# Kernel tuning notes

Measured on AMD Instinct MI355X. Metric: run time of the kernel, lower is better.

## Reference

```python
import jax, jax.numpy as jnp
import numpy as np

N_NODES = 100000
N_EDGES = 1600000
N_GRAPHS = 1000


def _gcn_layer(x, W, b, row, col, dinv):
    # GCNConv with improved=True: A_hat = A + 2I, symmetric normalization.
    xw = x @ W  # [N, out]
    norm = dinv[row] * dinv[col]  # [E]
    agg = jax.ops.segment_sum(norm[:, None] * xw[row], col, num_segments=N_NODES)
    # self-loop contribution with fill weight 2.0
    agg = agg + (2.0 * dinv * dinv)[:, None] * xw
    return agg + b


def setup_inputs() -> dict:
    key = jax.random.key(0)
    ks = jax.random.split(key, 20)
    x = jax.random.normal(ks[0], (N_NODES, 336), dtype=jnp.float32)
    edge_index = jax.random.randint(ks[1], (2, N_EDGES), 0, N_NODES, dtype=jnp.int64)
    batch = jnp.sort(jax.random.randint(ks[2], (N_NODES,), 0, N_GRAPHS, dtype=jnp.int64))
    def lin(k, din, dout):
        s = 1.0 / np.sqrt(din)
        return jax.random.uniform(k, (din, dout), jnp.float32, -s, s)
    params = {
        'W1': lin(ks[3], 336, 100), 'b1': jnp.zeros((100,), jnp.float32),
        'W2': lin(ks[4], 100, 100), 'b2': jnp.zeros((100,), jnp.float32),
        'W3': lin(ks[5], 100, 100), 'b3': jnp.zeros((100,), jnp.float32),
        'W4': lin(ks[6], 100, 100), 'b4': jnp.zeros((100,), jnp.float32),
        'W5': lin(ks[7], 100, 100), 'b5': jnp.zeros((100,), jnp.float32),
        'Wl1': lin(ks[8], 100, 100), 'bl1': jnp.zeros((100,), jnp.float32),
        'Wl2': lin(ks[9], 100, 100), 'bl2': jnp.zeros((100,), jnp.float32),
        'Wl3': lin(ks[10], 100, 29), 'bl3': jnp.zeros((29,), jnp.float32),
    }
    return {'x': x, 'edge_index': edge_index, 'batch': batch, **params}


def reference(x, edge_index, batch, W1, b1, W2, b2, W3, b3, W4, b4, W5, b5,
              Wl1, bl1, Wl2, bl2, Wl3, bl3):
    row, col = edge_index[0], edge_index[1]
    # degree of A + 2I (edge weights are 1, self-loop weight 2)
    deg = jax.ops.segment_sum(jnp.ones((N_EDGES,), x.dtype), col, num_segments=N_NODES) + 2.0
    dinv = deg ** -0.5
    h = jax.nn.relu(_gcn_layer(x, W1, b1, row, col, dinv))
    h = jax.nn.relu(_gcn_layer(h, W2, b2, row, col, dinv))
    h = jax.nn.relu(_gcn_layer(h, W3, b3, row, col, dinv))
    h = jax.nn.relu(_gcn_layer(h, W4, b4, row, col, dinv))
    h = jax.nn.relu(_gcn_layer(h, W5, b5, row, col, dinv))
    # global mean pool over graphs
    sums = jax.ops.segment_sum(h, batch, num_segments=N_GRAPHS)
    counts = jax.ops.segment_sum(jnp.ones((N_NODES,), h.dtype), batch, num_segments=N_GRAPHS)
    pooled = sums / jnp.maximum(counts, 1.0)[:, None]
    g = jax.nn.relu(pooled @ Wl1 + bl1)
    g = jax.nn.relu(g @ Wl2 + bl2)
    return g @ Wl3 + bl3
```

## Files before the change

kernel.cpp:

```cpp
#include <hip/hip_runtime.h>
#include <hip/hip_fp16.h>
#include <stdint.h>

#define NN 100000
#define NE 1600000
#define NG 1000
#define LDA 112
#define LDX 128

#define NPART 8
#define PRANGE 12500
#define SGRID 2048
#define PSTRIDE 65536

typedef float f32x4 __attribute__((ext_vector_type(4)));
typedef _Float16 f16x8 __attribute__((ext_vector_type(8)));

__device__ __forceinline__ void load_lds16(const void* g, void* l) {
    __builtin_amdgcn_global_load_lds((const __attribute__((address_space(1))) unsigned int*)g,
                                     (__attribute__((address_space(3))) unsigned int*)l,
                                     16, 0, 0);
}

__global__ void k_deg(const int* __restrict__ col, int* __restrict__ degcnt) {
    int part = blockIdx.x & (NPART - 1);
    int pb = blockIdx.x >> 3;
    int lo = part * PRANGE, hi = lo + PRANGE;
    for (int e = pb * 256 + threadIdx.x; e < NE; e += PSTRIDE) {
        int c = col[e];
        if (c >= lo && c < hi) atomicAdd(&degcnt[c], 1);
    }
}

__global__ void k_scan1(const int* __restrict__ cnt, int* __restrict__ csum) {
    __shared__ int s[256];
    int i = blockIdx.x * 256 + threadIdx.x;
    s[threadIdx.x] = (i < NN) ? cnt[i] : 0;
    __syncthreads();
    for (int o = 128; o > 0; o >>= 1) {
        if (threadIdx.x < o) s[threadIdx.x] += s[threadIdx.x + o];
        __syncthreads();
    }
    if (threadIdx.x == 0) csum[blockIdx.x] = s[0];
}

__global__ void k_scan2(const int* __restrict__ csum, int* __restrict__ csum2, int nb) {
    __shared__ int s[512];
    int t = threadIdx.x;
    int v = (t < nb) ? csum[t] : 0;
    s[t] = v; __syncthreads();
    for (int o = 1; o < 512; o <<= 1) {
        int x = (t >= o) ? s[t - o] : 0;
        __syncthreads();
        s[t] += x;
        __syncthreads();
    }
    if (t < nb) csum2[t] = s[t] - v;
}

__global__ void k_scan3d(const int* __restrict__ cnt, const int* __restrict__ csum2,
                         int* __restrict__ indptr, float* __restrict__ dinv) {
    __shared__ int s[256];
    int t = threadIdx.x;
    int i = blockIdx.x * 256 + t;
    int v = (i < NN) ? cnt[i] : 0;
    s[t] = v; __syncthreads();
    for (int o = 1; o < 256; o <<= 1) {
        int x = (t >= o) ? s[t - o] : 0;
        __syncthreads();
        s[t] += x;
        __syncthreads();
    }
    if (i < NN) {
        indptr[i] = csum2[blockIdx.x] + s[t] - v;
        dinv[i] = 1.0f / sqrtf((float)v + 2.0f);
    }
    if (i == 0) indptr[NN] = NE;
}

__global__ void k_scatter(const int* __restrict__ row, const int* __restrict__ col,
                          const int* __restrict__ indptr,
                          int* __restrict__ fill, int* __restrict__ esrc) {
    int part = blockIdx.x & (NPART - 1);
    int pb = blockIdx.x >> 3;
    int lo = part * PRANGE, hi = lo + PRANGE;
    for (int e = pb * 256 + threadIdx.x; e < NE; e += PSTRIDE) {
        int c = col[e];
        int r = row[e];
        if (c >= lo && c < hi) {
            int pos = indptr[c] + atomicAdd(&fill[c], 1);
            esrc[pos] = r;
        }
    }
}

__global__ void k_gbounds(const int* __restrict__ batch, int* __restrict__ gstart) {
    int i = blockIdx.x * 256 + threadIdx.x;
    if (i >= NN) return;
    int b = batch[i];
    int pb = (i == 0) ? -1 : batch[i - 1];
    for (int g = pb + 1; g <= b; g++) gstart[g] = i;
    if (i == NN - 1) {
        for (int g = b + 1; g <= NG; g++) gstart[g] = NN;
    }
}

__global__ void k_convW(const float* __restrict__ W1, __half* __restrict__ w1h, __half* __restrict__ w1l,
                        const float* __restrict__ W2, __half* __restrict__ w2h, __half* __restrict__ w2l,
                        const float* __restrict__ W3, __half* __restrict__ w3h, __half* __restrict__ w3l,
                        const float* __restrict__ W4, __half* __restrict__ w4h, __half* __restrict__ w4l,
                        const float* __restrict__ W5, __half* __restrict__ w5h, __half* __restrict__ w5l) {
    int b = blockIdx.x, t = threadIdx.x;
    const float* W; __half *Wh, *Wl; int K, KCP, idx;
    if (b < 168) {
        W = W1; Wh = w1h; Wl = w1l; K = 336; KCP = 384; idx = b * 256 + t;
    } else {
        int li = (b - 168) / 56;
        int lb = (b - 168) % 56;
        const float* Ws[4] = {W2, W3, W4, W5};
        __half* Whs[4] = {w2h, w3h, w4h, w5h};
        __half* Wls[4] = {w2l, w3l, w4l, w5l};
        W = Ws[li]; Wh = Whs[li]; Wl = Wls[li]; K = 100; KCP = 128; idx = lb * 256 + t;
    }
    int n = idx / KCP, k = idx - n * KCP;
    float v = (n < 100 && k < K) ? W[k * 100 + n] : 0.f;
    __half hi = __float2half(v);
    __half lo = __float2half((v - __half2float(hi)) * 2048.f);
    int kc = k & 127;
    size_t so = (size_t)n * KCP + (k - kc) + (kc ^ ((n & 7) << 3));
    Wh[so] = hi;
    Wl[so] = lo;
}

__device__ __forceinline__ f16x8 cvt8(float4 v0, float4 v1) {
    __half2 p0 = __floats2half2_rn(v0.x, v0.y);
    __half2 p1 = __floats2half2_rn(v0.z, v0.w);
    __half2 p2 = __floats2half2_rn(v1.x, v1.y);
    __half2 p3 = __floats2half2_rn(v1.z, v1.w);
    union { uint4 u; f16x8 f; } c;
    c.u.x = __builtin_bit_cast(unsigned, p0);
    c.u.y = __builtin_bit_cast(unsigned, p1);
    c.u.z = __builtin_bit_cast(unsigned, p2);
    c.u.w = __builtin_bit_cast(unsigned, p3);
    return c.f;
}

__global__ __launch_bounds__(512, 2) void k_gemmX(const float* __restrict__ x,
                                                  const __half* __restrict__ Whi,
                                                  const __half* __restrict__ Wlo,
                                                  const float* __restrict__ dinv,
                                                  __half* __restrict__ out) {
    __shared__ __align__(16) __half Hs[2][112 * 128];
    __shared__ __align__(16) __half Ls[2][112 * 128];
    int t = threadIdx.x;
    int lane = t & 63, wv = t >> 6;
    int l15 = lane & 15, quad = lane >> 4;
    int rowbase = blockIdx.x * 128;
    int arow = rowbase + wv * 16 + l15;
    bool arok = arow < NN;
    const float* xp = x + (size_t)arow * 336;

    f32x4 acch[7], accl[7];
#pragma unroll
    for (int i = 0; i < 7; i++)
#pragma unroll
        for (int r = 0; r < 4; r++) { acch[i][r] = 0.f; accl[i][r] = 0.f; }

    int swz = (l15 & 7) << 4;
    float4 araw[8];

    auto stage = [&](int buf, int k0) {
#pragma unroll
        for (int cch = 0; cch < 7; cch++) {
            int g = wv + cch * 8;
            int tb = (g >= 28);
            int o = (g - (tb ? 28 : 0)) * 1024 + lane * 16;
            int r = o >> 8, cc = o & 255;
            size_t src = (size_t)r * 768 + (size_t)(k0 * 2) + cc;
            if (!tb) load_lds16((const char*)Whi + src, (char*)Hs[buf] + o);
            else     load_lds16((const char*)Wlo + src, (char*)Ls[buf] + o);
        }
    };
    auto aload = [&](int k0) {
#pragma unroll
        for (int ks = 0; ks < 4; ks++) {
            int k = k0 + ks * 32 + quad * 8;
            float4 v0 = make_float4(0.f, 0.f, 0.f, 0.f), v1 = v0;
            if (arok && k < 336) {
                v0 = *(const float4*)(xp + k);
                v1 = *(const float4*)(xp + k + 4);
            }
            araw[ks * 2] = v0;
            araw[ks * 2 + 1] = v1;
        }
    };

    stage(0, 0);
    aload(0);

#pragma unroll
    for (int tch = 0; tch < 3; tch++) {
        asm volatile("s_waitcnt vmcnt(0)" ::: "memory");
        f16x8 a[4];
#pragma unroll
        for (int ks = 0; ks < 4; ks++) a[ks] = cvt8(araw[ks * 2], araw[ks * 2 + 1]);
        __builtin_amdgcn_s_barrier();
        __builtin_amdgcn_sched_barrier(0);
        if (tch < 2) {
            aload((tch + 1) * 128);
            stage((tch + 1) & 1, (tch + 1) * 128);
        }
        const char* HB = (const char*)Hs[tch & 1];
        const char* LB = (const char*)Ls[tch & 1];
#pragma unroll
        for (int ks = 0; ks < 4; ks++) {
            int cb = (ks * 64 + quad * 16) ^ swz;
#pragma unroll
            for (int tt = 0; tt < 7; tt++) {
                int ro = (tt * 16 + l15) * 256;
                f16x8 bh = *(const f16x8*)(HB + ro + cb);
                f16x8 bl = *(const f16x8*)(LB + ro + cb);
                acch[tt] = __builtin_amdgcn_mfma_f32_16x16x32_f16(a[ks], bh, acch[tt], 0, 0, 0);
                accl[tt] = __builtin_amdgcn_mfma_f32_16x16x32_f16(a[ks], bl, accl[tt], 0, 0, 0);
            }
        }
        __builtin_amdgcn_sched_barrier(0);
        __builtin_amdgcn_s_barrier();
    }

    int gr0 = rowbase + wv * 16 + quad * 4;
    float dv[4];
#pragma unroll
    for (int reg = 0; reg < 4; reg++) dv[reg] = (gr0 + reg < NN) ? dinv[gr0 + reg] : 0.f;
#pragma unroll
    for (int tt = 0; tt < 7; tt++) {
        int n = tt * 16 + l15;
#pragma unroll
        for (int reg = 0; reg < 4; reg++) {
            int gr = gr0 + reg;
            if (gr < NN)
                out[(size_t)gr * LDX + n] =
                    __float2half(dv[reg] * (acch[tt][reg] + accl[tt][reg] * (1.f / 2048.f)));
        }
    }
    if (l15 < 8) {
#pragma unroll
        for (int reg = 0; reg < 4; reg++) {
            int gr = gr0 + reg;
            if (gr < NN) *(unsigned int*)(out + (size_t)gr * LDX + 112 + l15 * 2) = 0u;
        }
    }
}

__global__ __launch_bounds__(512, 4) void k_gemmH(const __half* __restrict__ act,
                                                  const __half* __restrict__ Whi,
                                                  const __half* __restrict__ Wlo,
                                                  const float* __restrict__ dinv,
                                                  __half* __restrict__ out) {
    __shared__ __align__(16) __half Hs[112 * 128];
    __shared__ __align__(16) __half Ls[112 * 128];
    int t = threadIdx.x;
    int lane = t & 63, wv = t >> 6;
    int l15 = lane & 15, quad = lane >> 4;
    int rowbase = blockIdx.x * 128;
    int ar = min(rowbase + wv * 16 + l15, NN - 1);

    const char* ap = (const char*)act + (size_t)ar * 256;
    f16x8 a[4];
#pragma unroll
    for (int ks = 0; ks < 4; ks++)
        a[ks] = *(const f16x8*)(ap + ks * 64 + quad * 16);

#pragma unroll
    for (int cch = 0; cch < 7; cch++) {
        int g = wv + cch * 8;
        int tb = (g >= 28);
        int o = (g - (tb ? 28 : 0)) * 1024 + lane * 16;
        if (!tb) load_lds16((const char*)Whi + o, (char*)Hs + o);
        else     load_lds16((const char*)Wlo + o, (char*)Ls + o);
    }

    f32x4 acch[7], accl[7];
#pragma unroll
    for (int i = 0; i < 7; i++)
#pragma unroll
        for (int r = 0; r < 4; r++) { acch[i][r] = 0.f; accl[i][r] = 0.f; }

    __syncthreads();
    int swz = (l15 & 7) << 4;
#pragma unroll
    for (int ks = 0; ks < 4; ks++) {
        int cb = (ks * 64 + quad * 16) ^ swz;
#pragma unroll
        for (int tt = 0; tt < 7; tt++) {
            int ro = (tt * 16 + l15) * 256;
            f16x8 bh = *(const f16x8*)((const char*)Hs + ro + cb);
            f16x8 bl = *(const f16x8*)((const char*)Ls + ro + cb);
            acch[tt] = __builtin_amdgcn_mfma_f32_16x16x32_f16(a[ks], bh, acch[tt], 0, 0, 0);
            accl[tt] = __builtin_amdgcn_mfma_f32_16x16x32_f16(a[ks], bl, accl[tt], 0, 0, 0);
        }
    }

    int gr0 = rowbase + wv * 16 + quad * 4;
    float dv[4];
#pragma unroll
    for (int reg = 0; reg < 4; reg++) dv[reg] = (gr0 + reg < NN) ? dinv[gr0 + reg] : 0.f;
#pragma unroll
    for (int tt = 0; tt < 7; tt++) {
        int n = tt * 16 + l15;
#pragma unroll
        for (int reg = 0; reg < 4; reg++) {
            int gr = gr0 + reg;
            if (gr < NN)
                out[(size_t)gr * LDX + n] =
                    __float2half(dv[reg] * (acch[tt][reg] + accl[tt][reg] * (1.f / 2048.f)));
        }
    }
    if (l15 < 8) {
#pragma unroll
        for (int reg = 0; reg < 4; reg++) {
            int gr = gr0 + reg;
            if (gr < NN) *(unsigned int*)(out + (size_t)gr * LDX + 112 + l15 * 2) = 0u;
        }
    }
}

__device__ __forceinline__ void agg_core(const __half* __restrict__ xs,
                                         const int* __restrict__ esrc,
                                         int beg, int end, int lane, int col,
                                         float& ax, float& ay) {
    ax = 0.f; ay = 0.f;
    for (int c = beg; c < end; c += 64) {
        int m = min(64, end - c);
        int se = 0;
        if (lane < m) se = esrc[c + lane];
        int j = 0;
        for (; j + 32 <= m; j += 32) {
            __half2 v[32];
#pragma unroll
            for (int u = 0; u < 32; u++) {
                int s = __builtin_amdgcn_readlane(se, j + u);
                v[u] = *(const __half2*)(xs + (size_t)s * LDX + col);
            }
#pragma unroll
            for (int u = 0; u < 32; u++) {
                float2 f = __half22float2(v[u]);
                ax += f.x; ay += f.y;
            }
        }
        for (; j + 16 <= m; j += 16) {
            __half2 v[16];
#pragma unroll
            for (int u = 0; u < 16; u++) {
                int s = __builtin_amdgcn_readlane(se, j + u);
                v[u] = *(const __half2*)(xs + (size_t)s * LDX + col);
            }
#pragma unroll
            for (int u = 0; u < 16; u++) {
                float2 f = __half22float2(v[u]);
                ax += f.x; ay += f.y;
            }
        }
        for (; j + 8 <= m; j += 8) {
            __half2 v[8];
#pragma unroll
            for (int u = 0; u < 8; u++) {
                int s = __builtin_amdgcn_readlane(se, j + u);
                v[u] = *(const __half2*)(xs + (size_t)s * LDX + col);
            }
#pragma unroll
            for (int u = 0; u < 8; u++) {
                float2 f = __half22float2(v[u]);
                ax += f.x; ay += f.y;
            }
        }
        for (; j + 4 <= m; j += 4) {
            __half2 v[4];
#pragma unroll
            for (int u = 0; u < 4; u++) {
                int s = __builtin_amdgcn_readlane(se, j + u);
                v[u] = *(const __half2*)(xs + (size_t)s * LDX + col);
            }
#pragma unroll
            for (int u = 0; u < 4; u++) {
                float2 f = __half22float2(v[u]);
                ax += f.x; ay += f.y;
            }
        }
        for (; j < m; j++) {
            int s = __builtin_amdgcn_readlane(se, j);
            float2 f = __half22float2(*(const __half2*)(xs + (size_t)s * LDX + col));
            ax += f.x; ay += f.y;
        }
    }
}

__global__ __launch_bounds__(256) void k_aggS(const __half* __restrict__ xs,
                                              const int* __restrict__ indptr,
                                              const int* __restrict__ esrc,
                                              const float* __restrict__ dinv,
                                              const float* __restrict__ bias,
                                              __half* __restrict__ hh) {
    int wave = threadIdx.x >> 6;
    int lane = threadIdx.x & 63;
    int n = blockIdx.x * 4 + wave;
    if (n >= NN) return;
    int beg = indptr[n], end = indptr[n + 1];
    int col = (lane < 50) ? lane * 2 : 0;
    float ax, ay;
    agg_core(xs, esrc, beg, end, lane, col, ax, ay);
    if (lane < 50) {
        float di = dinv[n];
        float2 xv = __half22float2(*(const __half2*)(xs + (size_t)n * LDX + col));
        float2 bv = *(const float2*)(bias + lane * 2);
        float hx = fmaxf(di * (ax + 2.f * xv.x) + bv.x, 0.f);
        float hy = fmaxf(di * (ay + 2.f * xv.y) + bv.y, 0.f);
        *(__half2*)(hh + (size_t)n * LDX + col) = __floats2half2_rn(hx, hy);
    } else {
        int pc = 100 + (lane - 50) * 2;
        *(unsigned int*)(hh + (size_t)n * LDX + pc) = 0u;
    }
}

__global__ __launch_bounds__(256) void k_agg(const __half* __restrict__ xs,
                                             const int* __restrict__ indptr,
                                             const int* __restrict__ esrc,
                                             const float* __restrict__ dinv,
                                             const float* __restrict__ bias,
                                             float* __restrict__ hout) {
    int wave = threadIdx.x >> 6;
    int lane = threadIdx.x & 63;
    int n = blockIdx.x * 4 + wave;
    if (n >= NN) return;
    int beg = indptr[n], end = indptr[n + 1];
    int col = (lane < 50) ? lane * 2 : 0;
    float ax, ay;
    agg_core(xs, esrc, beg, end, lane, col, ax, ay);
    if (lane < 50) {
        float di = dinv[n];
        float2 xv = __half22float2(*(const __half2*)(xs + (size_t)n * LDX + col));
        float2 bv = *(const float2*)(bias + lane * 2);
        float2 r;
        r.x = fmaxf(di * (ax + 2.f * xv.x) + bv.x, 0.f);
        r.y = fmaxf(di * (ay + 2.f * xv.y) + bv.y, 0.f);
        *(float2*)(hout + (size_t)n * LDA + col) = r;
    }
}

__global__ __launch_bounds__(128) void k_pool(const float* __restrict__ h,
                                              const int* __restrict__ gstart,
                                              float* __restrict__ pooled) {
    int g = blockIdx.x, t = threadIdx.x;
    if (t >= 100) return;
    int st = gstart[g];
    int cnt = gstart[g + 1] - st;
    float s0 = 0.f, s1 = 0.f, s2 = 0.f, s3 = 0.f;
    float s4 = 0.f, s5 = 0.f, s6 = 0.f, s7 = 0.f;
    int i = 0;
    for (; i + 8 <= cnt; i += 8) {
        s0 += h[(size_t)(st + i) * LDA + t];
        s1 += h[(size_t)(st + i + 1) * LDA + t];
        s2 += h[(size_t)(st + i + 2) * LDA + t];
        s3 += h[(size_t)(st + i + 3) * LDA + t];
        s4 += h[(size_t)(st + i + 4) * LDA + t];
        s5 += h[(size_t)(st + i + 5) * LDA + t];
        s6 += h[(size_t)(st + i + 6) * LDA + t];
        s7 += h[(size_t)(st + i + 7) * LDA + t];
    }
    for (; i < cnt; i++) s0 += h[(size_t)(st + i) * LDA + t];
    float s = ((s0 + s1) + (s2 + s3)) + ((s4 + s5) + (s6 + s7));
    pooled[g * 100 + t] = s / (float)(cnt > 0 ? cnt : 1);
}

__global__ void k_mlp(const float* __restrict__ pooled,
                      const float* __restrict__ Wl1, const float* __restrict__ bl1,
                      const float* __restrict__ Wl2, const float* __restrict__ bl2,
                      const float* __restrict__ Wl3, const float* __restrict__ bl3,
                      float* __restrict__ out) {
    __shared__ float p[100], q[100];
    int g = blockIdx.x, t = threadIdx.x;
    if (t < 100) p[t] = pooled[g * 100 + t];
    __syncthreads();
    float s1 = 0.f;
    if (t < 100) {
        s1 = bl1[t];
        for (int k = 0; k < 100; k++) s1 += p[k] * Wl1[k * 100 + t];
        s1 = fmaxf(s1, 0.f);
    }
    __syncthreads();
    if (t < 100) q[t] = s1;
    __syncthreads();
    float s2 = 0.f;
    if (t < 100) {
        s2 = bl2[t];
        for (int k = 0; k < 100; k++) s2 += q[k] * Wl2[k * 100 + t];
        s2 = fmaxf(s2, 0.f);
    }
    __syncthreads();
    if (t < 100) p[t] = s2;
    __syncthreads();
    if (t < 29) {
        float s3 = bl3[t];
        for (int k = 0; k < 100; k++) s3 += p[k] * Wl3[k * 29 + t];
        out[g * 29 + t] = s3;
    }
}

extern "C" void kernel_launch(void* const* d_in, const int* in_sizes, int n_in,
                              void* d_out, int out_size, void* d_ws, size_t ws_size,
                              hipStream_t stream) {
    const float* x     = (const float*)d_in[0];
    const int*   ei    = (const int*)d_in[1];
    const int*   batch = (const int*)d_in[2];
    const float* W1 = (const float*)d_in[3];  const float* b1 = (const float*)d_in[4];
    const float* W2 = (const float*)d_in[5];  const float* b2 = (const float*)d_in[6];
    const float* W3 = (const float*)d_in[7];  const float* b3 = (const float*)d_in[8];
    const float* W4 = (const float*)d_in[9];  const float* b4 = (const float*)d_in[10];
    const float* W5 = (const float*)d_in[11]; const float* b5 = (const float*)d_in[12];
    const float* Wl1 = (const float*)d_in[13]; const float* bl1 = (const float*)d_in[14];
    const float* Wl2 = (const float*)d_in[15]; const float* bl2 = (const float*)d_in[16];
    const float* Wl3 = (const float*)d_in[17]; const float* bl3 = (const float*)d_in[18];
    float* out = (float*)d_out;

    const int* row = ei;
    const int* col = ei + NE;

    uintptr_t base = (uintptr_t)d_ws;
    auto alloc = [&](size_t bytes) -> void* {
        void* p = (void*)base;
        base += (bytes + 255) & ~(size_t)255;
        return p;
    };
    int*   cnts   = (int*)alloc((size_t)(2 * NN) * 4);
    int*   degcnt = cnts;
    int*   fill   = cnts + NN;
    float* dinv   = (float*)alloc(NN * 4);
    int*   indptr = (int*)alloc((NN + 1) * 4);
    int*   csum   = (int*)alloc(512 * 4);
    int*   csum2  = (int*)alloc(512 * 4);
    int*   gstart = (int*)alloc((NG + 1) * 4);
    int*   esrc   = (int*)alloc((size_t)NE * 4);
    __half* xsh   = (__half*)alloc((size_t)NN * LDX * 2);
    __half* hh    = (__half*)alloc((size_t)NN * LDX * 2);
    float* h      = (float*)alloc((size_t)NN * LDA * 4);
    float* pooled = (float*)alloc((size_t)NG * 100 * 4);
    __half* w1hi = (__half*)alloc((size_t)112 * 384 * 2);
    __half* w1lo = (__half*)alloc((size_t)112 * 384 * 2);
    __half* w2hi = (__half*)alloc((size_t)112 * 128 * 2);
    __half* w2lo = (__half*)alloc((size_t)112 * 128 * 2);
    __half* w3hi = (__half*)alloc((size_t)112 * 128 * 2);
    __half* w3lo = (__half*)alloc((size_t)112 * 128 * 2);
    __half* w4hi = (__half*)alloc((size_t)112 * 128 * 2);
    __half* w4lo = (__half*)alloc((size_t)112 * 128 * 2);
    __half* w5hi = (__half*)alloc((size_t)112 * 128 * 2);
    __half* w5lo = (__half*)alloc((size_t)112 * 128 * 2);

    hipMemsetAsync(cnts, 0, (size_t)(2 * NN) * 4, stream);

    const int NB = (NN + 255) / 256;
    k_deg<<<SGRID, 256, 0, stream>>>(col, degcnt);
    k_scan1<<<NB, 256, 0, stream>>>(degcnt, csum);
    k_scan2<<<1, 512, 0, stream>>>(csum, csum2, NB);
    k_scan3d<<<NB, 256, 0, stream>>>(degcnt, csum2, indptr, dinv);
    k_scatter<<<SGRID, 256, 0, stream>>>(row, col, indptr, fill, esrc);
    k_gbounds<<<NB, 256, 0, stream>>>(batch, gstart);
    k_convW<<<392, 256, 0, stream>>>(W1, w1hi, w1lo, W2, w2hi, w2lo,
                                     W3, w3hi, w3lo, W4, w4hi, w4lo,
                                     W5, w5hi, w5lo);

    const int GEMM_GRID = (NN + 127) / 128;
    const int AGG_GRID = (NN + 3) / 4;

    k_gemmX<<<GEMM_GRID, 512, 0, stream>>>(x, w1hi, w1lo, dinv, xsh);
    k_aggS<<<AGG_GRID, 256, 0, stream>>>(xsh, indptr, esrc, dinv, b1, hh);
    k_gemmH<<<GEMM_GRID, 512, 0, stream>>>(hh, w2hi, w2lo, dinv, xsh);
    k_aggS<<<AGG_GRID, 256, 0, stream>>>(xsh, indptr, esrc, dinv, b2, hh);
    k_gemmH<<<GEMM_GRID, 512, 0, stream>>>(hh, w3hi, w3lo, dinv, xsh);
    k_aggS<<<AGG_GRID, 256, 0, stream>>>(xsh, indptr, esrc, dinv, b3, hh);
    k_gemmH<<<GEMM_GRID, 512, 0, stream>>>(hh, w4hi, w4lo, dinv, xsh);
    k_aggS<<<AGG_GRID, 256, 0, stream>>>(xsh, indptr, esrc, dinv, b4, hh);
    k_gemmH<<<GEMM_GRID, 512, 0, stream>>>(hh, w5hi, w5lo, dinv, xsh);
    k_agg<<<AGG_GRID, 256, 0, stream>>>(xsh, indptr, esrc, dinv, b5, h);

    k_pool<<<NG, 128, 0, stream>>>(h, gstart, pooled);
    k_mlp<<<NG, 128, 0, stream>>>(pooled, Wl1, bl1, Wl2, bl2, Wl3, bl3, out);
}
```

Before: 835.5 us.

## Shrink weight tiles to 100 rows and drop double buffering to raise GEMM occupancy

Stores the transposed hi/lo fp16 weight tiles with 100 output rows instead of 112 padded rows, shrinking LDS per block. B-fragment reads clamp row indices past 99 and zero those output columns. k_gemmX drops its double-buffered LDS staging in favour of a single buffer loaded each K chunk, with a partial vmcnt wait so the next x chunk prefetches during compute. Launch bounds rise to 4 and 6 blocks per SM, aiming for more resident waves, at the cost of losing weight-load/compute overlap in k_gemmX and possibly more register pressure.

```diff
diff --git a/kernel.cpp b/kernel.cpp
--- a/kernel.cpp
+++ b/kernel.cpp
@@ -112,18 +112,18 @@
                         const float* __restrict__ W5, __half* __restrict__ w5h, __half* __restrict__ w5l) {
     int b = blockIdx.x, t = threadIdx.x;
     const float* W; __half *Wh, *Wl; int K, KCP, idx;
-    if (b < 168) {
+    if (b < 150) {
         W = W1; Wh = w1h; Wl = w1l; K = 336; KCP = 384; idx = b * 256 + t;
     } else {
-        int li = (b - 168) / 56;
-        int lb = (b - 168) % 56;
+        int li = (b - 150) / 50;
+        int lb = (b - 150) % 50;
         const float* Ws[4] = {W2, W3, W4, W5};
         __half* Whs[4] = {w2h, w3h, w4h, w5h};
         __half* Wls[4] = {w2l, w3l, w4l, w5l};
         W = Ws[li]; Wh = Whs[li]; Wl = Wls[li]; K = 100; KCP = 128; idx = lb * 256 + t;
     }
     int n = idx / KCP, k = idx - n * KCP;
-    float v = (n < 100 && k < K) ? W[k * 100 + n] : 0.f;
+    float v = (k < K) ? W[k * 100 + n] : 0.f;
     __half hi = __float2half(v);
     __half lo = __float2half((v - __half2float(hi)) * 2048.f);
     int kc = k & 127;
@@ -145,13 +145,13 @@
     return c.f;
 }
 
-__global__ __launch_bounds__(512, 2) void k_gemmX(const float* __restrict__ x,
+__global__ __launch_bounds__(512, 4) void k_gemmX(const float* __restrict__ x,
                                                   const __half* __restrict__ Whi,
                                                   const __half* __restrict__ Wlo,
                                                   const float* __restrict__ dinv,
                                                   __half* __restrict__ out) {
-    __shared__ __align__(16) __half Hs[2][112 * 128];
-    __shared__ __align__(16) __half Ls[2][112 * 128];
+    __shared__ __align__(16) __half Hs[100 * 128];
+    __shared__ __align__(16) __half Ls[100 * 128];
     int t = threadIdx.x;
     int lane = t & 63, wv = t >> 6;
     int l15 = lane & 15, quad = lane >> 4;
@@ -169,16 +169,18 @@
     int swz = (l15 & 7) << 4;
     float4 araw[8];
 
-    auto stage = [&](int buf, int k0) {
-#pragma unroll
-        for (int cch = 0; cch < 7; cch++) {
-            int g = wv + cch * 8;
-            int tb = (g >= 28);
-            int o = (g - (tb ? 28 : 0)) * 1024 + lane * 16;
-            int r = o >> 8, cc = o & 255;
-            size_t src = (size_t)r * 768 + (size_t)(k0 * 2) + cc;
-            if (!tb) load_lds16((const char*)Whi + src, (char*)Hs[buf] + o);
-            else     load_lds16((const char*)Wlo + src, (char*)Ls[buf] + o);
+    auto stage = [&](int k0) {
+#pragma unroll
+        for (int i = 0; i < 7; i++) {
+            int g = wv + i * 8;
+            if (g < 50) {
+                int tb = (g >= 25);
+                int o = (g - (tb ? 25 : 0)) * 1024 + lane * 16;
+                int r = o >> 8, cc = o & 255;
+                size_t src = (size_t)r * 768 + (size_t)(k0 * 2) + cc;
+                if (!tb) load_lds16((const char*)Whi + src, (char*)Hs + o);
+                else     load_lds16((const char*)Wlo + src, (char*)Ls + o);
+            }
         }
     };
     auto aload = [&](int k0) {
@@ -195,31 +197,33 @@
         }
     };
 
-    stage(0, 0);
     aload(0);
 
 #pragma unroll
     for (int tch = 0; tch < 3; tch++) {
-        asm volatile("s_waitcnt vmcnt(0)" ::: "memory");
+        stage(tch * 128);
         f16x8 a[4];
 #pragma unroll
         for (int ks = 0; ks < 4; ks++) a[ks] = cvt8(araw[ks * 2], araw[ks * 2 + 1]);
+        if (tch < 2) {
+            aload((tch + 1) * 128);
+            asm volatile("s_waitcnt vmcnt(8)" ::: "memory");
+        } else {
+            asm volatile("s_waitcnt vmcnt(0)" ::: "memory");
+        }
+        __builtin_amdgcn_sched_barrier(0);
         __builtin_amdgcn_s_barrier();
         __builtin_amdgcn_sched_barrier(0);
-        if (tch < 2) {
-            aload((tch + 1) * 128);
-            stage((tch + 1) & 1, (tch + 1) * 128);
-        }
-        const char* HB = (const char*)Hs[tch & 1];
-        const char* LB = (const char*)Ls[tch & 1];
 #pragma unroll
         for (int ks = 0; ks < 4; ks++) {
             int cb = (ks * 64 + quad * 16) ^ swz;
 #pragma unroll
             for (int tt = 0; tt < 7; tt++) {
-                int ro = (tt * 16 + l15) * 256;
-                f16x8 bh = *(const f16x8*)(HB + ro + cb);
-                f16x8 bl = *(const f16x8*)(LB + ro + cb);
+                int nrow = tt * 16 + l15;
+                int nr = (nrow > 99) ? 99 : nrow;
+                int ro = nr * 256;
+                f16x8 bh = *(const f16x8*)((const char*)Hs + ro + cb);
+                f16x8 bl = *(const f16x8*)((const char*)Ls + ro + cb);
                 acch[tt] = __builtin_amdgcn_mfma_f32_16x16x32_f16(a[ks], bh, acch[tt], 0, 0, 0);
                 accl[tt] = __builtin_amdgcn_mfma_f32_16x16x32_f16(a[ks], bl, accl[tt], 0, 0, 0);
             }
@@ -238,9 +242,10 @@
 #pragma unroll
         for (int reg = 0; reg < 4; reg++) {
             int gr = gr0 + reg;
-            if (gr < NN)
-                out[(size_t)gr * LDX + n] =
-                    __float2half(dv[reg] * (acch[tt][reg] + accl[tt][reg] * (1.f / 2048.f)));
+            if (gr < NN) {
+                float v = dv[reg] * (acch[tt][reg] + accl[tt][reg] * (1.f / 2048.f));
+                out[(size_t)gr * LDX + n] = (n < 100) ? __float2half(v) : __half(0.f);
+            }
         }
     }
     if (l15 < 8) {
@@ -252,13 +257,13 @@
     }
 }
 
-__global__ __launch_bounds__(512, 4) void k_gemmH(const __half* __restrict__ act,
+__global__ __launch_bounds__(512, 6) void k_gemmH(const __half* __restrict__ act,
                                                   const __half* __restrict__ Whi,
                                                   const __half* __restrict__ Wlo,
                                                   const float* __restrict__ dinv,
                                                   __half* __restrict__ out) {
-    __shared__ __align__(16) __half Hs[112 * 128];
-    __shared__ __align__(16) __half Ls[112 * 128];
+    __shared__ __align__(16) __half Hs[100 * 128];
+    __shared__ __align__(16) __half Ls[100 * 128];
     int t = threadIdx.x;
     int lane = t & 63, wv = t >> 6;
     int l15 = lane & 15, quad = lane >> 4;
@@ -272,12 +277,14 @@
         a[ks] = *(const f16x8*)(ap + ks * 64 + quad * 16);
 
 #pragma unroll
-    for (int cch = 0; cch < 7; cch++) {
-        int g = wv + cch * 8;
-        int tb = (g >= 28);
-        int o = (g - (tb ? 28 : 0)) * 1024 + lane * 16;
-        if (!tb) load_lds16((const char*)Whi + o, (char*)Hs + o);
-        else     load_lds16((const char*)Wlo + o, (char*)Ls + o);
+    for (int i = 0; i < 7; i++) {
+        int g = wv + i * 8;
+        if (g < 50) {
+            int tb = (g >= 25);
+            int o = (g - (tb ? 25 : 0)) * 1024 + lane * 16;
+            if (!tb) load_lds16((const char*)Whi + o, (char*)Hs + o);
+            else     load_lds16((const char*)Wlo + o, (char*)Ls + o);
+        }
     }
 
     f32x4 acch[7], accl[7];
@@ -293,7 +300,9 @@
         int cb = (ks * 64 + quad * 16) ^ swz;
 #pragma unroll
         for (int tt = 0; tt < 7; tt++) {
-            int ro = (tt * 16 + l15) * 256;
+            int nrow = tt * 16 + l15;
+            int nr = (nrow > 99) ? 99 : nrow;
+            int ro = nr * 256;
             f16x8 bh = *(const f16x8*)((const char*)Hs + ro + cb);
             f16x8 bl = *(const f16x8*)((const char*)Ls + ro + cb);
             acch[tt] = __builtin_amdgcn_mfma_f32_16x16x32_f16(a[ks], bh, acch[tt], 0, 0, 0);
@@ -311,9 +320,10 @@
 #pragma unroll
         for (int reg = 0; reg < 4; reg++) {
             int gr = gr0 + reg;
-            if (gr < NN)
-                out[(size_t)gr * LDX + n] =
-                    __float2half(dv[reg] * (acch[tt][reg] + accl[tt][reg] * (1.f / 2048.f)));
+            if (gr < NN) {
+                float v = dv[reg] * (acch[tt][reg] + accl[tt][reg] * (1.f / 2048.f));
+                out[(size_t)gr * LDX + n] = (n < 100) ? __float2half(v) : __half(0.f);
+            }
         }
     }
     if (l15 < 8) {
@@ -544,16 +554,16 @@
     __half* hh    = (__half*)alloc((size_t)NN * LDX * 2);
     float* h      = (float*)alloc((size_t)NN * LDA * 4);
     float* pooled = (float*)alloc((size_t)NG * 100 * 4);
-    __half* w1hi = (__half*)alloc((size_t)112 * 384 * 2);
-    __half* w1lo = (__half*)alloc((size_t)112 * 384 * 2);
-    __half* w2hi = (__half*)alloc((size_t)112 * 128 * 2);
-    __half* w2lo = (__half*)alloc((size_t)112 * 128 * 2);
-    __half* w3hi = (__half*)alloc((size_t)112 * 128 * 2);
-    __half* w3lo = (__half*)alloc((size_t)112 * 128 * 2);
-    __half* w4hi = (__half*)alloc((size_t)112 * 128 * 2);
-    __half* w4lo = (__half*)alloc((size_t)112 * 128 * 2);
-    __half* w5hi = (__half*)alloc((size_t)112 * 128 * 2);
-    __half* w5lo = (__half*)alloc((size_t)112 * 128 * 2);
+    __half* w1hi = (__half*)alloc((size_t)100 * 384 * 2);
+    __half* w1lo = (__half*)alloc((size_t)100 * 384 * 2);
+    __half* w2hi = (__half*)alloc((size_t)100 * 128 * 2);
+    __half* w2lo = (__half*)alloc((size_t)100 * 128 * 2);
+    __half* w3hi = (__half*)alloc((size_t)100 * 128 * 2);
+    __half* w3lo = (__half*)alloc((size_t)100 * 128 * 2);
+    __half* w4hi = (__half*)alloc((size_t)100 * 128 * 2);
+    __half* w4lo = (__half*)alloc((size_t)100 * 128 * 2);
+    __half* w5hi = (__half*)alloc((size_t)100 * 128 * 2);
+    __half* w5lo = (__half*)alloc((size_t)100 * 128 * 2);
 
     hipMemsetAsync(cnts, 0, (size_t)(2 * NN) * 4, stream);
 
@@ -564,7 +574,7 @@
     k_scan3d<<<NB, 256, 0, stream>>>(degcnt, csum2, indptr, dinv);
     k_scatter<<<SGRID, 256, 0, stream>>>(row, col, indptr, fill, esrc);
     k_gbounds<<<NB, 256, 0, stream>>>(batch, gstart);
-    k_convW<<<392, 256, 0, stream>>>(W1, w1hi, w1lo, W2, w2hi, w2lo,
+    k_convW<<<350, 256, 0, stream>>>(W1, w1hi, w1lo, W2, w2hi, w2lo,
                                      W3, w3hi, w3lo, W4, w4hi, w4lo,
                                      W5, w5hi, w5lo);
 
```

Measured after the change: 883.7 us. 1.06x slower.
